# Kernel optimization log

Measured on AMD Instinct MI355X. Metric: run time of the kernel, lower is better.

Reference implementation:

```python
import jax, jax.numpy as jnp
import numpy as np

NUM_ENT = 50000
NUM_REL = 500
DIM = 128
BATCH = 32
INIT_RHO = -5.0


def setup_inputs() -> dict:
    key = jax.random.key(0)
    k1, k2, k3 = jax.random.split(key, 3)
    ent_center = jax.random.uniform(k1, (NUM_ENT, 2 * DIM), minval=-0.1, maxval=0.1, dtype=jnp.float32)
    ent_rho = jnp.full((NUM_ENT, DIM), INIT_RHO, dtype=jnp.float32)
    rel_center = jax.random.uniform(k2, (NUM_REL, DIM), minval=-np.pi, maxval=np.pi, dtype=jnp.float32)
    rel_rho = jnp.full((NUM_REL, DIM), INIT_RHO, dtype=jnp.float32)
    pos_triplets = jax.random.randint(k3, (BATCH, 3), 0, NUM_REL, dtype=jnp.int64)
    return {
        "ent_center": ent_center,
        "ent_rho": ent_rho,
        "rel_center": rel_center,
        "rel_rho": rel_rho,
        "pos_triplets": pos_triplets,
    }


def reference(ent_center, ent_rho, rel_center, rel_rho, pos_triplets):
    # All-entity embeddings: center split into (re, im) halves, radius via softplus.
    u_re, u_im = jnp.split(ent_center, 2, axis=-1)          # [N, D] each
    u_r = jax.nn.softplus(ent_rho)                           # [N, D]

    h_idx = pos_triplets[:, 0]
    r_idx = pos_triplets[:, 1]

    hc = ent_center[h_idx]                                   # [B, 2D]
    hr = jax.nn.softplus(ent_rho[h_idx])                     # [B, D]
    rc_phase = rel_center[r_idx]                             # [B, D]
    rr = jax.nn.softplus(rel_rho[r_idx])                     # [B, D]

    hc_re, hc_im = jnp.split(hc, 2, axis=-1)                 # [B, D]
    cos_r = jnp.cos(rc_phase)
    sin_r = jnp.sin(rc_phase)
    pred_re = hc_re * cos_r - hc_im * sin_r                  # [B, D]
    pred_im = hc_re * sin_r + hc_im * cos_r                  # [B, D]
    pred_r = hr + rr                                         # [B, D]

    # Broadcast L2 (complex magnitude) distance to every entity: [B, N]
    diff_re = pred_re[:, None, :] - u_re[None, :, :]         # [B, N, D]
    diff_im = pred_im[:, None, :] - u_im[None, :, :]         # [B, N, D]
    dist_c = jnp.sqrt(diff_re ** 2 + diff_im ** 2).sum(axis=-1)  # [B, N]

    # sum over dim of (pred_r + u_r) broadcast == sum(pred_r) + sum(u_r)
    sum_r = pred_r.sum(axis=-1)[:, None] + u_r.sum(axis=-1)[None, :]  # [B, N]
    return sum_r - dist_c
```

## Files before the change

### kernel.cpp

```cpp
#include <hip/hip_runtime.h>
#include <math.h>

#define NENT 50000
#define NREL 500
#define DIMK 128
#define BATCH 32

#define WS_PRED_FLOATS (BATCH * DIMK * 2)

__device__ __forceinline__ float softplus_f(float x) {
    float e = __expf(-fabsf(x));
    return fmaxf(x, 0.0f) + __logf(1.0f + e);
}

__device__ __forceinline__ float fast_sqrtf(float x) {
#if __has_builtin(__builtin_amdgcn_sqrtf)
    return __builtin_amdgcn_sqrtf(x);
#else
    return sqrtf(x);
#endif
}

__device__ __forceinline__ int get_idx(const void* trip, int flat) {
    const long long* t64 = (const long long*)trip;
    const int* t32 = (const int*)trip;
    bool is64 = true;
    #pragma unroll 1
    for (int i = 0; i < 48; ++i) {
        long long v = t64[i];
        if (v < 0 || v >= NREL) { is64 = false; break; }
    }
    return is64 ? (int)t64[flat] : t32[flat];
}

__global__ __launch_bounds__(128)
void prep_kernel(const float* __restrict__ ent_center,
                 const float* __restrict__ ent_rho,
                 const float* __restrict__ rel_center,
                 const float* __restrict__ rel_rho,
                 const void* __restrict__ trip,
                 float* __restrict__ ws) {
    const int b = blockIdx.x;
    const int d = threadIdx.x;
    const int h = get_idx(trip, b * 3 + 0);
    const int r = get_idx(trip, b * 3 + 1);

    float hre = ent_center[h * 256 + d];
    float him = ent_center[h * 256 + 128 + d];
    float ph  = rel_center[r * 128 + d];
    float s = sinf(ph), c = cosf(ph);
    float pre = hre * c - him * s;
    float pim = hre * s + him * c;
    ws[(b * 128 + d) * 2 + 0] = pre;
    ws[(b * 128 + d) * 2 + 1] = pim;

    float pr = softplus_f(ent_rho[h * 128 + d]) + softplus_f(rel_rho[r * 128 + d]);
    #pragma unroll
    for (int off = 32; off > 0; off >>= 1) pr += __shfl_down(pr, off);
    __shared__ float tmp[2];
    if ((threadIdx.x & 63) == 0) tmp[threadIdx.x >> 6] = pr;
    __syncthreads();
    if (threadIdx.x == 0) ws[WS_PRED_FLOATS + b] = tmp[0] + tmp[1];
}

__global__ __launch_bounds__(256, 2)
void score_kernel(const float* __restrict__ ent_center,
                  const float* __restrict__ ent_rho,
                  const float* __restrict__ ws,
                  float* __restrict__ out) {
    __shared__ float s_pred[WS_PRED_FLOATS];
    __shared__ float s_psum[BATCH];
    __shared__ float s_red[3 * 64 * 33];

    const int tid = threadIdx.x;
    {
        const float4* wsv = (const float4*)ws;
        float4* sp4 = (float4*)s_pred;
        #pragma unroll
        for (int i = 0; i < 8; ++i) sp4[tid + 256 * i] = wsv[tid + 256 * i];
        if (tid < BATCH) s_psum[tid] = ws[WS_PRED_FLOATS + tid];
    }
    __syncthreads();

    const int wave = tid >> 6, lane = tid & 63;
    const int e = blockIdx.x * 64 + lane;
    const int ec = (e < NENT) ? e : (NENT - 1);
    const float4* cen = (const float4*)(ent_center + (size_t)ec * 256);
    const float4* rho = (const float4*)(ent_rho + (size_t)ec * 128);
    const int qbase = wave * 8;

    float acc[BATCH];
    #pragma unroll
    for (int b = 0; b < BATCH; ++b) acc[b] = 0.0f;
    float ursum = 0.0f;

    #pragma unroll 1
    for (int dc = 0; dc < 8; ++dc) {
        const int dq = qbase + dc;
        float4 ur = cen[dq];
        float4 ui = cen[32 + dq];
        float4 rr = rho[dq];
        ursum += softplus_f(rr.x) + softplus_f(rr.y) + softplus_f(rr.z) + softplus_f(rr.w);

        const float* pbase = s_pred + dq * 8;
        #pragma unroll
        for (int b = 0; b < BATCH; ++b) {
            const float4* p = (const float4*)(pbase + b * 256);
            float4 p01 = p[0];
            float4 p23 = p[1];
            float dre, dim_, t;
            dre = p01.x - ur.x; dim_ = p01.y - ui.x; t = dre * dre + dim_ * dim_; acc[b] += fast_sqrtf(t);
            dre = p01.z - ur.y; dim_ = p01.w - ui.y; t = dre * dre + dim_ * dim_; acc[b] += fast_sqrtf(t);
            dre = p23.x - ur.z; dim_ = p23.y - ui.z; t = dre * dre + dim_ * dim_; acc[b] += fast_sqrtf(t);
            dre = p23.z - ur.w; dim_ = p23.w - ui.w; t = dre * dre + dim_ * dim_; acc[b] += fast_sqrtf(t);
        }
    }

    if (wave > 0) {
        float* rp = s_red + ((wave - 1) * 64 + lane) * 33;
        #pragma unroll
        for (int b = 0; b < BATCH; ++b) rp[b] = acc[b];
        rp[32] = ursum;
    }
    __syncthreads();

    if (wave == 0 && e < NENT) {
        #pragma unroll
        for (int k = 0; k < 3; ++k) {
            const float* rp = s_red + (k * 64 + lane) * 33;
            #pragma unroll
            for (int b = 0; b < BATCH; ++b) acc[b] += rp[b];
            ursum += rp[32];
        }
        #pragma unroll
        for (int b = 0; b < BATCH; ++b)
            out[(size_t)b * NENT + e] = s_psum[b] + ursum - acc[b];
    }
}

extern "C" void kernel_launch(void* const* d_in, const int* in_sizes, int n_in,
                              void* d_out, int out_size, void* d_ws, size_t ws_size,
                              hipStream_t stream) {
    const float* ent_center = (const float*)d_in[0];
    const float* ent_rho    = (const float*)d_in[1];
    const float* rel_center = (const float*)d_in[2];
    const float* rel_rho    = (const float*)d_in[3];
    const void*  trip       = d_in[4];
    float* ws  = (float*)d_ws;
    float* out = (float*)d_out;

    prep_kernel<<<BATCH, 128, 0, stream>>>(ent_center, ent_rho, rel_center, rel_rho, trip, ws);
    score_kernel<<<(NENT + 63) / 64, 256, 0, stream>>>(ent_center, ent_rho, ws, out);
}
```

Measured before the change: 184.1 us.

## Stage entity tiles in LDS, split batch across waves, precompute rho sums

The score kernel now splits work by batch instead of by dimension. Each wave handles 8 batch rows over all 128 dims, which removes the cross-wave LDS reduction and cuts the per-thread accumulators from 32 to 8. Entity center rows are loaded cooperatively with coalesced float4 loads, double-buffered through registers into an XOR-swizzled LDS stage. The entity softplus row sums move to a separate ursum kernel that writes them to the workspace. This adds a third launch and extra syncthreads per chunk, in exchange for better occupancy (launch bounds raised to 3) and a simpler epilogue.

```diff
diff --git a/kernel.cpp b/kernel.cpp
--- a/kernel.cpp
+++ b/kernel.cpp
@@ -6,7 +6,9 @@
 #define DIMK 128
 #define BATCH 32
 
-#define WS_PRED_FLOATS (BATCH * DIMK * 2)
+#define WS_PRED 0
+#define WS_PSUM 8192
+#define WS_URSUM 8224
 
 __device__ __forceinline__ float softplus_f(float x) {
     float e = __expf(-fabsf(x));
@@ -49,10 +51,8 @@
     float him = ent_center[h * 256 + 128 + d];
     float ph  = rel_center[r * 128 + d];
     float s = sinf(ph), c = cosf(ph);
-    float pre = hre * c - him * s;
-    float pim = hre * s + him * c;
-    ws[(b * 128 + d) * 2 + 0] = pre;
-    ws[(b * 128 + d) * 2 + 1] = pim;
+    ws[WS_PRED + (b * 128 + d) * 2 + 0] = hre * c - him * s;
+    ws[WS_PRED + (b * 128 + d) * 2 + 1] = hre * s + him * c;
 
     float pr = softplus_f(ent_rho[h * 128 + d]) + softplus_f(rel_rho[r * 128 + d]);
     #pragma unroll
@@ -60,81 +60,99 @@
     __shared__ float tmp[2];
     if ((threadIdx.x & 63) == 0) tmp[threadIdx.x >> 6] = pr;
     __syncthreads();
-    if (threadIdx.x == 0) ws[WS_PRED_FLOATS + b] = tmp[0] + tmp[1];
+    if (threadIdx.x == 0) ws[WS_PSUM + b] = tmp[0] + tmp[1];
 }
 
-__global__ __launch_bounds__(256, 2)
+__global__ __launch_bounds__(256)
+void ursum_kernel(const float* __restrict__ ent_rho, float* __restrict__ ws) {
+    const int wave = threadIdx.x >> 6, lane = threadIdx.x & 63;
+    const int e = blockIdx.x * 4 + wave;
+    if (e >= NENT) return;
+    float2 v = *(const float2*)(ent_rho + (size_t)e * 128 + lane * 2);
+    float s = softplus_f(v.x) + softplus_f(v.y);
+    #pragma unroll
+    for (int off = 32; off > 0; off >>= 1) s += __shfl_down(s, off);
+    if (lane == 0) ws[WS_URSUM + e] = s;
+}
+
+__global__ __launch_bounds__(256, 3)
 void score_kernel(const float* __restrict__ ent_center,
-                  const float* __restrict__ ent_rho,
                   const float* __restrict__ ws,
                   float* __restrict__ out) {
-    __shared__ float s_pred[WS_PRED_FLOATS];
-    __shared__ float s_psum[BATCH];
-    __shared__ float s_red[3 * 64 * 33];
+    __shared__ float4 s_pred[2048];
+    __shared__ float4 s_stage[1024];
 
     const int tid = threadIdx.x;
-    {
-        const float4* wsv = (const float4*)ws;
-        float4* sp4 = (float4*)s_pred;
+    const int wave = tid >> 6, lane = tid & 63;
+    const int e0 = blockIdx.x * 64;
+    const int q = tid & 7;
+    const int et0 = tid >> 3;
+    const float4* cen4 = (const float4*)ent_center;
+    const float4* ws4 = (const float4*)ws;
+
+    #pragma unroll
+    for (int i = 0; i < 8; ++i) s_pred[tid + 256 * i] = ws4[tid + 256 * i];
+
+    float4 g[4];
+    auto GLOAD = [&](int c) {
         #pragma unroll
-        for (int i = 0; i < 8; ++i) sp4[tid + 256 * i] = wsv[tid + 256 * i];
-        if (tid < BATCH) s_psum[tid] = ws[WS_PRED_FLOATS + tid];
-    }
+        for (int s = 0; s < 2; ++s)
+            #pragma unroll
+            for (int r = 0; r < 2; ++r) {
+                int ge = e0 + et0 + 32 * r;
+                if (ge > NENT - 1) ge = NENT - 1;
+                g[s * 2 + r] = cen4[(size_t)ge * 64 + s * 32 + c * 8 + q];
+            }
+    };
+    auto DSWRITE = [&]() {
+        #pragma unroll
+        for (int s = 0; s < 2; ++s)
+            #pragma unroll
+            for (int r = 0; r < 2; ++r) {
+                int et = et0 + 32 * r;
+                s_stage[(s * 8 + q) * 64 + (et ^ q)] = g[s * 2 + r];
+            }
+    };
+
+    float acc[8];
+    #pragma unroll
+    for (int b = 0; b < 8; ++b) acc[b] = 0.0f;
+
+    GLOAD(0);
     __syncthreads();
-
-    const int wave = tid >> 6, lane = tid & 63;
-    const int e = blockIdx.x * 64 + lane;
-    const int ec = (e < NENT) ? e : (NENT - 1);
-    const float4* cen = (const float4*)(ent_center + (size_t)ec * 256);
-    const float4* rho = (const float4*)(ent_rho + (size_t)ec * 128);
-    const int qbase = wave * 8;
-
-    float acc[BATCH];
-    #pragma unroll
-    for (int b = 0; b < BATCH; ++b) acc[b] = 0.0f;
-    float ursum = 0.0f;
-
     #pragma unroll 1
-    for (int dc = 0; dc < 8; ++dc) {
-        const int dq = qbase + dc;
-        float4 ur = cen[dq];
-        float4 ui = cen[32 + dq];
-        float4 rr = rho[dq];
-        ursum += softplus_f(rr.x) + softplus_f(rr.y) + softplus_f(rr.z) + softplus_f(rr.w);
-
-        const float* pbase = s_pred + dq * 8;
+    for (int c = 0; c < 4; ++c) {
+        if (c) __syncthreads();
+        DSWRITE();
+        if (c < 3) GLOAD(c + 1);
+        __syncthreads();
         #pragma unroll
-        for (int b = 0; b < BATCH; ++b) {
-            const float4* p = (const float4*)(pbase + b * 256);
-            float4 p01 = p[0];
-            float4 p23 = p[1];
-            float dre, dim_, t;
-            dre = p01.x - ur.x; dim_ = p01.y - ui.x; t = dre * dre + dim_ * dim_; acc[b] += fast_sqrtf(t);
-            dre = p01.z - ur.y; dim_ = p01.w - ui.y; t = dre * dre + dim_ * dim_; acc[b] += fast_sqrtf(t);
-            dre = p23.x - ur.z; dim_ = p23.y - ui.z; t = dre * dre + dim_ * dim_; acc[b] += fast_sqrtf(t);
-            dre = p23.z - ur.w; dim_ = p23.w - ui.w; t = dre * dre + dim_ * dim_; acc[b] += fast_sqrtf(t);
+        for (int dq = 0; dq < 8; ++dq) {
+            const float4 ur = s_stage[dq * 64 + (lane ^ dq)];
+            const float4 ui = s_stage[(8 + dq) * 64 + (lane ^ dq)];
+            #pragma unroll
+            for (int bb = 0; bb < 8; ++bb) {
+                const int b = wave * 8 + bb;
+                const int p0 = b * 64 + c * 16 + dq * 2;
+                const float4 p01 = s_pred[p0];
+                const float4 p23 = s_pred[p0 + 1];
+                float dre, dmi, t;
+                dre = p01.x - ur.x; dmi = p01.y - ui.x; t = dre * dre + dmi * dmi; acc[bb] += fast_sqrtf(t);
+                dre = p01.z - ur.y; dmi = p01.w - ui.y; t = dre * dre + dmi * dmi; acc[bb] += fast_sqrtf(t);
+                dre = p23.x - ur.z; dmi = p23.y - ui.z; t = dre * dre + dmi * dmi; acc[bb] += fast_sqrtf(t);
+                dre = p23.z - ur.w; dmi = p23.w - ui.w; t = dre * dre + dmi * dmi; acc[bb] += fast_sqrtf(t);
+            }
         }
     }
 
-    if (wave > 0) {
-        float* rp = s_red + ((wave - 1) * 64 + lane) * 33;
+    const int e = e0 + lane;
+    if (e < NENT) {
+        const float ursum = ws[WS_URSUM + e];
         #pragma unroll
-        for (int b = 0; b < BATCH; ++b) rp[b] = acc[b];
-        rp[32] = ursum;
-    }
-    __syncthreads();
-
-    if (wave == 0 && e < NENT) {
-        #pragma unroll
-        for (int k = 0; k < 3; ++k) {
-            const float* rp = s_red + (k * 64 + lane) * 33;
-            #pragma unroll
-            for (int b = 0; b < BATCH; ++b) acc[b] += rp[b];
-            ursum += rp[32];
+        for (int bb = 0; bb < 8; ++bb) {
+            const int b = wave * 8 + bb;
+            out[(size_t)b * NENT + e] = ws[WS_PSUM + b] + ursum - acc[bb];
         }
-        #pragma unroll
-        for (int b = 0; b < BATCH; ++b)
-            out[(size_t)b * NENT + e] = s_psum[b] + ursum - acc[b];
     }
 }
 
@@ -149,6 +167,7 @@
     float* ws  = (float*)d_ws;
     float* out = (float*)d_out;
 
+    ursum_kernel<<<(NENT + 3) / 4, 256, 0, stream>>>(ent_rho, ws);
     prep_kernel<<<BATCH, 128, 0, stream>>>(ent_center, ent_rho, rel_center, rel_rho, trip, ws);
-    score_kernel<<<(NENT + 63) / 64, 256, 0, stream>>>(ent_center, ent_rho, ws, out);
+    score_kernel<<<(NENT + 63) / 64, 256, 0, stream>>>(ent_center, ws, out);
 }
```

After: 160.1 us. 1.15x faster.
